# Kernel tuning notes

Hardware: AMD Instinct MI355X
Metric: run time of the kernel (lower is better)

## Reference

```python
import jax, jax.numpy as jnp
import numpy as np

B, L, D, H = 4, 2048, 1024, 16
HD = D // H

def setup_inputs() -> dict:
    key = jax.random.key(0)
    k1, k2, k3, k4 = jax.random.split(key, 4)
    return {
        "Q": jax.random.normal(k1, (B, L, D), dtype=jnp.float32),
        "K": jax.random.normal(k2, (B, L, D), dtype=jnp.float32),
        "V": jax.random.normal(k3, (B, L, D), dtype=jnp.float32),
        "W_out": jax.random.normal(k4, (D, D), dtype=jnp.float32) * (1.0 / np.sqrt(D)),
        "b_out": jnp.zeros((D,), dtype=jnp.float32),
    }

def reference(Q, K, V, W_out, b_out):
    b, l, d = Q.shape
    h, hd = H, d // H
    q = Q.reshape(b, l, h, hd)
    k = K.reshape(b, l, h, hd)
    v = V.reshape(b, l, h, hd)
    # energy: [b, h, q, k]
    energy = jnp.einsum('nqhd,nkhd->nhqk', q, k)
    # NOTE: original scales by sqrt(embed_dim), not sqrt(head_dim)
    attn = jax.nn.softmax(energy / jnp.sqrt(jnp.float32(d)), axis=-1)
    out = jnp.einsum('nhql,nlhd->nqhd', attn, v).reshape(b, l, d)
    # torch nn.Linear: x @ W.T + b
    return out @ W_out.T + b_out
```

## Files before the change

### kernel.cpp

```cpp
#include <hip/hip_runtime.h>
#include <hip/hip_bf16.h>


#define B_  4
#define L_  2048
#define D_  1024
#define H_  16
#define HD_ 64

typedef float  f32x4  __attribute__((ext_vector_type(4)));
typedef short  bf16x8 __attribute__((ext_vector_type(8)));
typedef short  bf16x4 __attribute__((ext_vector_type(4)));

__device__ inline unsigned short f2bf(float x) {
    union { float f; unsigned u; } v; v.f = x;
    unsigned r = v.u + 0x7FFFu + ((v.u >> 16) & 1u);
    return (unsigned short)(r >> 16);
}
__device__ inline unsigned short f2bf_trunc(float x) {
    union { float f; unsigned u; } v; v.f = x;
    return (unsigned short)(v.u >> 16);
}
__device__ inline unsigned pack_trunc2(float lo, float hi) {
    union { float f; unsigned u; } a, b; a.f = lo; b.f = hi;
    return (a.u >> 16) | (b.u & 0xFFFF0000u);
}
__device__ inline float fast_exp2(float x) {
#if __has_builtin(__builtin_amdgcn_exp2f)
    return __builtin_amdgcn_exp2f(x);
#else
    return exp2f(x);
#endif
}
__device__ inline bf16x8 pack8s(float4 a, float4 b, float s) {
    bf16x8 r;
    r[0] = (short)f2bf(a.x * s); r[1] = (short)f2bf(a.y * s);
    r[2] = (short)f2bf(a.z * s); r[3] = (short)f2bf(a.w * s);
    r[4] = (short)f2bf(b.x * s); r[5] = (short)f2bf(b.y * s);
    r[6] = (short)f2bf(b.z * s); r[7] = (short)f2bf(b.w * s);
    return r;
}
__device__ inline void gld16(const void* g, void* l) {
    __builtin_amdgcn_global_load_lds(
        (const __attribute__((address_space(1))) void*)g,
        (__attribute__((address_space(3))) void*)l, 16, 0, 0);
}

__global__ __launch_bounds__(256) void convw_kernel(const float* __restrict__ W,
                                                    unsigned short* __restrict__ Wb) {
    int i = (blockIdx.x * 256 + threadIdx.x) * 4;
    float4 v = *(const float4*)&W[i];
    bf16x4 o;
    o[0] = (short)f2bf(v.x); o[1] = (short)f2bf(v.y);
    o[2] = (short)f2bf(v.z); o[3] = (short)f2bf(v.w);
    *(bf16x4*)&Wb[i] = o;
}

__global__ __launch_bounds__(256, 4) void attn_kernel(const float* __restrict__ Qg,
                                                      const float* __restrict__ Kg,
                                                      const float* __restrict__ Vg,
                                                      unsigned short* __restrict__ Og) {
    __shared__ unsigned short Ks[64 * 72];
    __shared__ unsigned short Vt[64 * 72];
    __shared__ unsigned short Pw[4 * 32 * 72];

    const int tid  = threadIdx.x;
    const int w    = tid >> 6;
    const int lane = tid & 63;
    const int l16  = lane & 15;
    const int quad = lane >> 4;

    const int x   = blockIdx.x;
    const int idx = x >> 3;
    const int bh  = (x & 7) * 8 + (idx & 7);
    const int qb  = idx >> 3;
    const int bz  = bh >> 4;
    const int h   = bh & 15;
    const int q0  = qb * 128;

    const float qscale = 0.04508422f;
    bf16x8 aq[2][2];
    #pragma unroll
    for (int qt = 0; qt < 2; ++qt) {
        const int qrow = q0 + w * 32 + qt * 16 + l16;
        const float* qp = Qg + ((size_t)(bz * L_ + qrow)) * D_ + h * HD_ + quad * 8;
        aq[qt][0] = pack8s(*(const float4*)qp,        *(const float4*)(qp + 4),  qscale);
        aq[qt][1] = pack8s(*(const float4*)(qp + 32), *(const float4*)(qp + 36), qscale);
    }

    f32x4 o[2][4];
    float lsum[2][4];
    #pragma unroll
    for (int qt = 0; qt < 2; ++qt)
        #pragma unroll
        for (int i = 0; i < 4; ++i) {
            o[qt][i] = (f32x4){0.f, 0.f, 0.f, 0.f};
            lsum[qt][i] = 0.f;
        }

    for (int k0 = 0; k0 < L_; k0 += 64) {
        __syncthreads();
        #pragma unroll
        for (int i = 0; i < 4; ++i) {
            int fi  = i * 256 + tid;
            int row = fi >> 4, c4 = fi & 15;
            const float* kp = Kg + ((size_t)(bz * L_ + k0 + row)) * D_ + h * HD_ + c4 * 4;
            float4 kv = *(const float4*)kp;
            bf16x4 kb;
            kb[0] = (short)f2bf(kv.x); kb[1] = (short)f2bf(kv.y);
            kb[2] = (short)f2bf(kv.z); kb[3] = (short)f2bf(kv.w);
            *(bf16x4*)&Ks[row * 72 + c4 * 4] = kb;
        }
        {
            int kp2 = tid & 31, dg = tid >> 5;
            const float* vp = Vg + ((size_t)(bz * L_ + k0 + 2 * kp2)) * D_ + h * HD_ + dg * 8;
            float4 a0 = *(const float4*)vp,        a1 = *(const float4*)(vp + 4);
            float4 b0 = *(const float4*)(vp + D_), b1 = *(const float4*)(vp + D_ + 4);
            const float* aa = (const float*)&a0;
            const float* bb = (const float*)&b0;
            #pragma unroll
            for (int j = 0; j < 4; ++j) {
                *(unsigned*)&Vt[(dg * 8 + j) * 72 + 2 * kp2]       = pack_trunc2(a0[j==0?0:j==1?1:j==2?2:3], b0[j==0?0:j==1?1:j==2?2:3]);
            }
            #pragma unroll
            for (int j = 0; j < 4; ++j) {
                *(unsigned*)&Vt[(dg * 8 + 4 + j) * 72 + 2 * kp2]   = pack_trunc2(((const float*)&a1)[j], ((const float*)&b1)[j]);
            }
            (void)aa; (void)bb;
        }
        __syncthreads();

        #pragma unroll
        for (int qt = 0; qt < 2; ++qt) {
            f32x4 s[4];
            #pragma unroll
            for (int i = 0; i < 4; ++i) s[i] = (f32x4){0.f, 0.f, 0.f, 0.f};
            #pragma unroll
            for (int nt = 0; nt < 4; ++nt)
                #pragma unroll
                for (int ks = 0; ks < 2; ++ks) {
                    bf16x8 kb = *(const bf16x8*)&Ks[(nt * 16 + l16) * 72 + ks * 32 + quad * 8];
                    s[nt] = __builtin_amdgcn_mfma_f32_16x16x32_bf16(aq[qt][ks], kb, s[nt], 0, 0, 0);
                }
            #pragma unroll
            for (int nt = 0; nt < 4; ++nt)
                #pragma unroll
                for (int r = 0; r < 4; ++r) {
                    float p = fast_exp2(s[nt][r]);
                    lsum[qt][r] += p;
                    Pw[(w * 32 + qt * 16 + quad * 4 + r) * 72 + nt * 16 + l16] = f2bf_trunc(p);
                }
        }
        #pragma unroll
        for (int qt = 0; qt < 2; ++qt) {
            bf16x8 pa0 = *(const bf16x8*)&Pw[(w * 32 + qt * 16 + l16) * 72 + quad * 8];
            bf16x8 pa1 = *(const bf16x8*)&Pw[(w * 32 + qt * 16 + l16) * 72 + 32 + quad * 8];
            #pragma unroll
            for (int dt = 0; dt < 4; ++dt) {
                bf16x8 v0 = *(const bf16x8*)&Vt[(dt * 16 + l16) * 72 + quad * 8];
                bf16x8 v1 = *(const bf16x8*)&Vt[(dt * 16 + l16) * 72 + 32 + quad * 8];
                o[qt][dt] = __builtin_amdgcn_mfma_f32_16x16x32_bf16(pa0, v0, o[qt][dt], 0, 0, 0);
                o[qt][dt] = __builtin_amdgcn_mfma_f32_16x16x32_bf16(pa1, v1, o[qt][dt], 0, 0, 0);
            }
        }
    }

    #pragma unroll
    for (int qt = 0; qt < 2; ++qt)
        #pragma unroll
        for (int r = 0; r < 4; ++r) {
            float v = lsum[qt][r];
            #pragma unroll
            for (int m = 1; m < 16; m <<= 1) v += __shfl_xor(v, m);
            lsum[qt][r] = v;
        }

    #pragma unroll
    for (int qt = 0; qt < 2; ++qt)
        #pragma unroll
        for (int r = 0; r < 4; ++r) {
            float inv = 1.0f / lsum[qt][r];
            int q = q0 + w * 32 + qt * 16 + quad * 4 + r;
            #pragma unroll
            for (int dt = 0; dt < 4; ++dt)
                Og[((size_t)(bz * L_ + q)) * D_ + h * HD_ + dt * 16 + l16] =
                    f2bf(o[qt][dt][r] * inv);
        }
}

__global__ __launch_bounds__(256, 2) void proj_kernel(const unsigned short* __restrict__ Og,
                                                      const unsigned short* __restrict__ Wb,
                                                      const float* __restrict__ bias,
                                                      float* __restrict__ Yg) {
    __shared__ unsigned short As[128 * 32];
    __shared__ unsigned short Bs[128 * 32];

    const int tid  = threadIdx.x;
    const int w    = tid >> 6;
    const int lane = tid & 63;
    const int l16  = lane & 15;
    const int quad = lane >> 4;
    const int wm   = w & 1, wn = w >> 1;

    const int m0 = blockIdx.x * 128;
    const int n0 = blockIdx.y * 128;

    f32x4 acc[4][4];
    #pragma unroll
    for (int i = 0; i < 4; ++i)
        #pragma unroll
        for (int j = 0; j < 4; ++j) acc[i][j] = (f32x4){0.f, 0.f, 0.f, 0.f};

    for (int kt = 0; kt < 1024; kt += 32) {
        __syncthreads();
        #pragma unroll
        for (int i = 0; i < 2; ++i) {
            int c   = (i * 4 + w) * 64 + lane;
            int row = c >> 2, q4 = c & 3;
            gld16(&Og[(size_t)(m0 + row) * 1024 + kt + q4 * 8],
                  (char*)As + (size_t)(i * 4 + w) * 1024);
            gld16(&Wb[(size_t)(n0 + row) * 1024 + kt + q4 * 8],
                  (char*)Bs + (size_t)(i * 4 + w) * 1024);
        }
        __syncthreads();

        bf16x8 a[4], b[4];
        #pragma unroll
        for (int mt = 0; mt < 4; ++mt)
            a[mt] = *(const bf16x8*)&As[(wm * 64 + mt * 16 + l16) * 32 + quad * 8];
        #pragma unroll
        for (int nt = 0; nt < 4; ++nt)
            b[nt] = *(const bf16x8*)&Bs[(wn * 64 + nt * 16 + l16) * 32 + quad * 8];
        #pragma unroll
        for (int mt = 0; mt < 4; ++mt)
            #pragma unroll
            for (int nt = 0; nt < 4; ++nt)
                acc[mt][nt] = __builtin_amdgcn_mfma_f32_16x16x32_bf16(a[mt], b[nt], acc[mt][nt], 0, 0, 0);
    }

    #pragma unroll
    for (int mt = 0; mt < 4; ++mt)
        #pragma unroll
        for (int nt = 0; nt < 4; ++nt) {
            int e = n0 + wn * 64 + nt * 16 + l16;
            float bv = bias[e];
            #pragma unroll
            for (int r = 0; r < 4; ++r) {
                int m = m0 + wm * 64 + mt * 16 + quad * 4 + r;
                Yg[(size_t)m * 1024 + e] = acc[mt][nt][r] + bv;
            }
        }
}

extern "C" void kernel_launch(void* const* d_in, const int* in_sizes, int n_in,
                              void* d_out, int out_size, void* d_ws, size_t ws_size,
                              hipStream_t stream) {
    const float* Q    = (const float*)d_in[0];
    const float* K    = (const float*)d_in[1];
    const float* V    = (const float*)d_in[2];
    const float* W    = (const float*)d_in[3];
    const float* bias = (const float*)d_in[4];
    float* Y = (float*)d_out;

    unsigned short* Og = (unsigned short*)d_ws;
    unsigned short* Wb = (unsigned short*)((char*)d_ws + (size_t)16 * 1024 * 1024);

    convw_kernel<<<D_ * D_ / (256 * 4), 256, 0, stream>>>(W, Wb);
    attn_kernel<<<B_ * H_ * (L_ / 128), 256, 0, stream>>>(Q, K, V, Og);
    dim3 pg(B_ * L_ / 128, D_ / 128);
    proj_kernel<<<pg, 256, 0, stream>>>(Og, Wb, bias, Y);
}
```

Baseline: 287.6 us.

## Preconvert K/V to swizzled bf16 and double-buffer async LDS loads in attention and projection

Adds prepass kernels that convert K to bf16 with an XOR-swizzled layout and V to a transposed, swizzled bf16 layout, staged in the output buffer as scratch. The attention kernel then streams these tiles with global_load_lds into double-buffered, unpadded LDS, overlapping the next tile's load with compute and dropping one barrier per iteration. It also computes S transposed so the row sum reduces with fewer shuffles and P is written as packed pairs. The projection GEMM gets the same double buffering. This removes the per-block fp32 to bf16 conversion of K/V, which was repeated for every query block, at the cost of extra prepass launches and extra global traffic.

```diff
diff --git a/kernel.cpp b/kernel.cpp
--- a/kernel.cpp
+++ b/kernel.cpp
@@ -6,7 +6,6 @@
 #define L_  2048
 #define D_  1024
 #define H_  16
-#define HD_ 64
 
 typedef float  f32x4  __attribute__((ext_vector_type(4)));
 typedef short  bf16x8 __attribute__((ext_vector_type(8)));
@@ -17,9 +16,8 @@
     unsigned r = v.u + 0x7FFFu + ((v.u >> 16) & 1u);
     return (unsigned short)(r >> 16);
 }
-__device__ inline unsigned short f2bf_trunc(float x) {
-    union { float f; unsigned u; } v; v.f = x;
-    return (unsigned short)(v.u >> 16);
+__device__ inline unsigned pack_rne2(float lo, float hi) {
+    return (unsigned)f2bf(lo) | ((unsigned)f2bf(hi) << 16);
 }
 __device__ inline unsigned pack_trunc2(float lo, float hi) {
     union { float f; unsigned u; } a, b; a.f = lo; b.f = hi;
@@ -56,13 +54,54 @@
     *(bf16x4*)&Wb[i] = o;
 }
 
-__global__ __launch_bounds__(256, 4) void attn_kernel(const float* __restrict__ Qg,
-                                                      const float* __restrict__ Kg,
-                                                      const float* __restrict__ Vg,
+__global__ __launch_bounds__(256) void convk_kernel(const float* __restrict__ K,
+                                                    unsigned short* __restrict__ Kb) {
+    int o = blockIdx.x * 256 + threadIdx.x;
+    int d8 = o & 7; int h = (o >> 3) & 15; int key = (o >> 7) & 2047; int b = o >> 18;
+    size_t base = ((size_t)(b * L_ + key) * H_ + h) * 64;
+    const float* p = K + base + d8 * 8;
+    float4 a = *(const float4*)p, c = *(const float4*)(p + 4);
+    bf16x8 r;
+    r[0] = (short)f2bf(a.x); r[1] = (short)f2bf(a.y); r[2] = (short)f2bf(a.z); r[3] = (short)f2bf(a.w);
+    r[4] = (short)f2bf(c.x); r[5] = (short)f2bf(c.y); r[6] = (short)f2bf(c.z); r[7] = (short)f2bf(c.w);
+    *(bf16x8*)&Kb[base + ((d8 * 8) ^ ((key & 7) * 8))] = r;
+}
+
+__global__ __launch_bounds__(256) void convv_kernel(const float* __restrict__ V,
+                                                    unsigned short* __restrict__ Vb) {
+    __shared__ unsigned short T[64 * 80];
+    int tid = threadIdx.x;
+    int kb_ = blockIdx.x & 31, bh = blockIdx.x >> 5;
+    int b = bh >> 4, h = bh & 15, k0 = kb_ * 64;
+    int key2 = tid & 31, dg = tid >> 5;
+    const float* pa = V + ((size_t)(b * L_ + k0 + 2 * key2) * H_ + h) * 64 + dg * 8;
+    const float* pb = pa + H_ * 64;
+    float4 a0 = *(const float4*)pa, a1 = *(const float4*)(pa + 4);
+    float4 b0 = *(const float4*)pb, b1 = *(const float4*)(pb + 4);
+    #pragma unroll
+    for (int j = 0; j < 4; ++j)
+        *(unsigned*)&T[(dg * 8 + j) * 80 + 2 * key2] =
+            pack_rne2(((const float*)&a0)[j], ((const float*)&b0)[j]);
+    #pragma unroll
+    for (int j = 0; j < 4; ++j)
+        *(unsigned*)&T[(dg * 8 + 4 + j) * 80 + 2 * key2] =
+            pack_rne2(((const float*)&a1)[j], ((const float*)&b1)[j]);
+    __syncthreads();
+    #pragma unroll
+    for (int i = 0; i < 2; ++i) {
+        int c = i * 256 + tid; int d = c >> 3, ch = c & 7;
+        bf16x8 v = *(const bf16x8*)&T[d * 80 + ch * 8];
+        *(bf16x8*)&Vb[((size_t)(b * H_ + h) * 64 + d) * L_ + k0 + ((ch ^ (d & 7)) * 8)] = v;
+    }
+}
+
+__global__ __launch_bounds__(256, 3) void attn_kernel(const float* __restrict__ Qg,
+                                                      const unsigned short* __restrict__ Kb,
+                                                      const unsigned short* __restrict__ Vb,
                                                       unsigned short* __restrict__ Og) {
-    __shared__ unsigned short Ks[64 * 72];
-    __shared__ unsigned short Vt[64 * 72];
-    __shared__ unsigned short Pw[4 * 32 * 72];
+    __shared__ unsigned short Ks[2][64 * 64];
+    __shared__ unsigned short Vt[2][64 * 64];
+    __shared__ unsigned short Pw[4][32 * 64];
 
     const int tid  = threadIdx.x;
     const int w    = tid >> 6;
@@ -83,108 +122,108 @@
     #pragma unroll
     for (int qt = 0; qt < 2; ++qt) {
         const int qrow = q0 + w * 32 + qt * 16 + l16;
-        const float* qp = Qg + ((size_t)(bz * L_ + qrow)) * D_ + h * HD_ + quad * 8;
+        const float* qp = Qg + ((size_t)(bz * L_ + qrow)) * D_ + h * 64 + quad * 8;
         aq[qt][0] = pack8s(*(const float4*)qp,        *(const float4*)(qp + 4),  qscale);
         aq[qt][1] = pack8s(*(const float4*)(qp + 32), *(const float4*)(qp + 36), qscale);
     }
 
     f32x4 o[2][4];
-    float lsum[2][4];
+    float lsum[2] = {0.f, 0.f};
     #pragma unroll
     for (int qt = 0; qt < 2; ++qt)
         #pragma unroll
-        for (int i = 0; i < 4; ++i) {
-            o[qt][i] = (f32x4){0.f, 0.f, 0.f, 0.f};
-            lsum[qt][i] = 0.f;
-        }
-
-    for (int k0 = 0; k0 < L_; k0 += 64) {
+        for (int i = 0; i < 4; ++i) o[qt][i] = (f32x4){0.f, 0.f, 0.f, 0.f};
+
+    const unsigned short* Kbh = Kb + ((size_t)bz * L_ * H_ + h) * 64;
+    const unsigned short* Vbh = Vb + (size_t)(bz * H_ + h) * 64 * L_;
+    unsigned short* PwF = &Pw[0][0];
+    const int sw = (l16 & 7) * 8;
+
+    #define ISSUE(T, BUF)                                                           \
+        {                                                                           \
+            int k0_ = (T) * 64;                                                     \
+            _Pragma("unroll")                                                       \
+            for (int i = 0; i < 2; ++i) {                                           \
+                int c = i * 256 + tid; int rr = c >> 3, jj = c & 7;                 \
+                gld16(Kbh + (size_t)(k0_ + rr) * (H_ * 64) + jj * 8,                \
+                      (char*)Ks[BUF] + (i * 256 + w * 64) * 16);                    \
+                gld16(Vbh + (size_t)rr * L_ + k0_ + jj * 8,                         \
+                      (char*)Vt[BUF] + (i * 256 + w * 64) * 16);                    \
+            }                                                                       \
+        }
+
+    ISSUE(0, 0)
+
+    for (int t = 0; t < 32; ++t) {
         __syncthreads();
-        #pragma unroll
-        for (int i = 0; i < 4; ++i) {
-            int fi  = i * 256 + tid;
-            int row = fi >> 4, c4 = fi & 15;
-            const float* kp = Kg + ((size_t)(bz * L_ + k0 + row)) * D_ + h * HD_ + c4 * 4;
-            float4 kv = *(const float4*)kp;
-            bf16x4 kb;
-            kb[0] = (short)f2bf(kv.x); kb[1] = (short)f2bf(kv.y);
-            kb[2] = (short)f2bf(kv.z); kb[3] = (short)f2bf(kv.w);
-            *(bf16x4*)&Ks[row * 72 + c4 * 4] = kb;
-        }
-        {
-            int kp2 = tid & 31, dg = tid >> 5;
-            const float* vp = Vg + ((size_t)(bz * L_ + k0 + 2 * kp2)) * D_ + h * HD_ + dg * 8;
-            float4 a0 = *(const float4*)vp,        a1 = *(const float4*)(vp + 4);
-            float4 b0 = *(const float4*)(vp + D_), b1 = *(const float4*)(vp + D_ + 4);
-            const float* aa = (const float*)&a0;
-            const float* bb = (const float*)&b0;
-            #pragma unroll
-            for (int j = 0; j < 4; ++j) {
-                *(unsigned*)&Vt[(dg * 8 + j) * 72 + 2 * kp2]       = pack_trunc2(a0[j==0?0:j==1?1:j==2?2:3], b0[j==0?0:j==1?1:j==2?2:3]);
+        if (t < 31) ISSUE(t + 1, (t + 1) & 1)
+        const unsigned short* ks = Ks[t & 1];
+        const unsigned short* vt = Vt[t & 1];
+
+        f32x4 s[2][4];
+        #pragma unroll
+        for (int nt = 0; nt < 4; ++nt) {
+            bf16x8 k0f = *(const bf16x8*)&ks[(nt * 16 + l16) * 64 + ((quad * 8) ^ sw)];
+            bf16x8 k1f = *(const bf16x8*)&ks[(nt * 16 + l16) * 64 + ((32 + quad * 8) ^ sw)];
+            #pragma unroll
+            for (int qt = 0; qt < 2; ++qt) {
+                f32x4 z = (f32x4){0.f, 0.f, 0.f, 0.f};
+                z = __builtin_amdgcn_mfma_f32_16x16x32_bf16(k0f, aq[qt][0], z, 0, 0, 0);
+                s[qt][nt] = __builtin_amdgcn_mfma_f32_16x16x32_bf16(k1f, aq[qt][1], z, 0, 0, 0);
             }
-            #pragma unroll
-            for (int j = 0; j < 4; ++j) {
-                *(unsigned*)&Vt[(dg * 8 + 4 + j) * 72 + 2 * kp2]   = pack_trunc2(((const float*)&a1)[j], ((const float*)&b1)[j]);
+        }
+
+        #pragma unroll
+        for (int qt = 0; qt < 2; ++qt) {
+            int prow = (w * 32 + qt * 16 + l16) * 64;
+            #pragma unroll
+            for (int nt = 0; nt < 4; ++nt) {
+                float p0 = fast_exp2(s[qt][nt][0]), p1 = fast_exp2(s[qt][nt][1]);
+                float p2 = fast_exp2(s[qt][nt][2]), p3 = fast_exp2(s[qt][nt][3]);
+                lsum[qt] += (p0 + p1) + (p2 + p3);
+                int cb = nt * 16 + quad * 4;
+                *(unsigned*)&PwF[prow + ((cb)     ^ sw)] = pack_trunc2(p0, p1);
+                *(unsigned*)&PwF[prow + ((cb + 2) ^ sw)] = pack_trunc2(p2, p3);
             }
-            (void)aa; (void)bb;
-        }
-        __syncthreads();
-
+        }
+
+        bf16x8 pav[2][2];
         #pragma unroll
         for (int qt = 0; qt < 2; ++qt) {
-            f32x4 s[4];
-            #pragma unroll
-            for (int i = 0; i < 4; ++i) s[i] = (f32x4){0.f, 0.f, 0.f, 0.f};
-            #pragma unroll
-            for (int nt = 0; nt < 4; ++nt)
-                #pragma unroll
-                for (int ks = 0; ks < 2; ++ks) {
-                    bf16x8 kb = *(const bf16x8*)&Ks[(nt * 16 + l16) * 72 + ks * 32 + quad * 8];
-                    s[nt] = __builtin_amdgcn_mfma_f32_16x16x32_bf16(aq[qt][ks], kb, s[nt], 0, 0, 0);
-                }
-            #pragma unroll
-            for (int nt = 0; nt < 4; ++nt)
-                #pragma unroll
-                for (int r = 0; r < 4; ++r) {
-                    float p = fast_exp2(s[nt][r]);
-                    lsum[qt][r] += p;
-                    Pw[(w * 32 + qt * 16 + quad * 4 + r) * 72 + nt * 16 + l16] = f2bf_trunc(p);
-                }
-        }
-        #pragma unroll
-        for (int qt = 0; qt < 2; ++qt) {
-            bf16x8 pa0 = *(const bf16x8*)&Pw[(w * 32 + qt * 16 + l16) * 72 + quad * 8];
-            bf16x8 pa1 = *(const bf16x8*)&Pw[(w * 32 + qt * 16 + l16) * 72 + 32 + quad * 8];
-            #pragma unroll
-            for (int dt = 0; dt < 4; ++dt) {
-                bf16x8 v0 = *(const bf16x8*)&Vt[(dt * 16 + l16) * 72 + quad * 8];
-                bf16x8 v1 = *(const bf16x8*)&Vt[(dt * 16 + l16) * 72 + 32 + quad * 8];
-                o[qt][dt] = __builtin_amdgcn_mfma_f32_16x16x32_bf16(pa0, v0, o[qt][dt], 0, 0, 0);
-                o[qt][dt] = __builtin_amdgcn_mfma_f32_16x16x32_bf16(pa1, v1, o[qt][dt], 0, 0, 0);
+            int prow = (w * 32 + qt * 16 + l16) * 64;
+            pav[qt][0] = *(const bf16x8*)&PwF[prow + ((quad * 8)      ^ sw)];
+            pav[qt][1] = *(const bf16x8*)&PwF[prow + ((32 + quad * 8) ^ sw)];
+        }
+        #pragma unroll
+        for (int dt = 0; dt < 4; ++dt) {
+            bf16x8 v0 = *(const bf16x8*)&vt[(dt * 16 + l16) * 64 + ((quad * 8)      ^ sw)];
+            bf16x8 v1 = *(const bf16x8*)&vt[(dt * 16 + l16) * 64 + ((32 + quad * 8) ^ sw)];
+            #pragma unroll
+            for (int qt = 0; qt < 2; ++qt) {
+                o[qt][dt] = __builtin_amdgcn_mfma_f32_16x16x32_bf16(pav[qt][0], v0, o[qt][dt], 0, 0, 0);
+                o[qt][dt] = __builtin_amdgcn_mfma_f32_16x16x32_bf16(pav[qt][1], v1, o[qt][dt], 0, 0, 0);
             }
         }
     }
 
+    float tot[2];
+    #pragma unroll
+    for (int qt = 0; qt < 2; ++qt) {
+        float v = lsum[qt];
+        v += __shfl_xor(v, 16); v += __shfl_xor(v, 32);
+        tot[qt] = v;
+    }
     #pragma unroll
     for (int qt = 0; qt < 2; ++qt)
         #pragma unroll
         for (int r = 0; r < 4; ++r) {
-            float v = lsum[qt][r];
-            #pragma unroll
-            for (int m = 1; m < 16; m <<= 1) v += __shfl_xor(v, m);
-            lsum[qt][r] = v;
-        }
-
-    #pragma unroll
-    for (int qt = 0; qt < 2; ++qt)
-        #pragma unroll
-        for (int r = 0; r < 4; ++r) {
-            float inv = 1.0f / lsum[qt][r];
+            float tv  = __shfl(tot[qt], quad * 4 + r);
+            float inv = 1.0f / tv;
             int q = q0 + w * 32 + qt * 16 + quad * 4 + r;
+            size_t rowb = ((size_t)(bz * L_ + q)) * D_ + h * 64;
             #pragma unroll
             for (int dt = 0; dt < 4; ++dt)
-                Og[((size_t)(bz * L_ + q)) * D_ + h * HD_ + dt * 16 + l16] =
-                    f2bf(o[qt][dt][r] * inv);
+                Og[rowb + dt * 16 + l16] = f2bf(o[qt][dt][r] * inv);
         }
 }
 
@@ -192,8 +231,8 @@
                                                       const unsigned short* __restrict__ Wb,
                                                       const float* __restrict__ bias,
                                                       float* __restrict__ Yg) {
-    __shared__ unsigned short As[128 * 32];
-    __shared__ unsigned short Bs[128 * 32];
+    __shared__ unsigned short As[2][128 * 32];
+    __shared__ unsigned short Bs[2][128 * 32];
 
     const int tid  = threadIdx.x;
     const int w    = tid >> 6;
@@ -211,26 +250,34 @@
         #pragma unroll
         for (int j = 0; j < 4; ++j) acc[i][j] = (f32x4){0.f, 0.f, 0.f, 0.f};
 
-    for (int kt = 0; kt < 1024; kt += 32) {
+    #define PISSUE(T, BUF)                                                          \
+        {                                                                           \
+            int kt_ = (T) * 32;                                                     \
+            _Pragma("unroll")                                                       \
+            for (int i = 0; i < 2; ++i) {                                           \
+                int c = i * 256 + tid; int row = c >> 2, q4 = c & 3;                \
+                gld16(&Og[(size_t)(m0 + row) * 1024 + kt_ + q4 * 8],                \
+                      (char*)As[BUF] + (i * 256 + w * 64) * 16);                    \
+                gld16(&Wb[(size_t)(n0 + row) * 1024 + kt_ + q4 * 8],                \
+                      (char*)Bs[BUF] + (i * 256 + w * 64) * 16);                    \
+            }                                                                       \
+        }
+
+    PISSUE(0, 0)
+
+    for (int t = 0; t < 32; ++t) {
         __syncthreads();
-        #pragma unroll
-        for (int i = 0; i < 2; ++i) {
-            int c   = (i * 4 + w) * 64 + lane;
-            int row = c >> 2, q4 = c & 3;
-            gld16(&Og[(size_t)(m0 + row) * 1024 + kt + q4 * 8],
-                  (char*)As + (size_t)(i * 4 + w) * 1024);
-            gld16(&Wb[(size_t)(n0 + row) * 1024 + kt + q4 * 8],
-                  (char*)Bs + (size_t)(i * 4 + w) * 1024);
-        }
-        __syncthreads();
+        if (t < 31) PISSUE(t + 1, (t + 1) & 1)
+        const unsigned short* as = As[t & 1];
+        const unsigned short* bs = Bs[t & 1];
 
         bf16x8 a[4], b[4];
         #pragma unroll
         for (int mt = 0; mt < 4; ++mt)
-            a[mt] = *(const bf16x8*)&As[(wm * 64 + mt * 16 + l16) * 32 + quad * 8];
+            a[mt] = *(const bf16x8*)&as[(wm * 64 + mt * 16 + l16) * 32 + quad * 8];
         #pragma unroll
         for (int nt = 0; nt < 4; ++nt)
-            b[nt] = *(const bf16x8*)&Bs[(wn * 64 + nt * 16 + l16) * 32 + quad * 8];
+            b[nt] = *(const bf16x8*)&bs[(wn * 64 + nt * 16 + l16) * 32 + quad * 8];
         #pragma unroll
         for (int mt = 0; mt < 4; ++mt)
             #pragma unroll
@@ -264,9 +311,13 @@
 
     unsigned short* Og = (unsigned short*)d_ws;
     unsigned short* Wb = (unsigned short*)((char*)d_ws + (size_t)16 * 1024 * 1024);
+    unsigned short* Kb = (unsigned short*)d_out;
+    unsigned short* Vb = Kb + (size_t)B_ * H_ * L_ * 64;
 
     convw_kernel<<<D_ * D_ / (256 * 4), 256, 0, stream>>>(W, Wb);
-    attn_kernel<<<B_ * H_ * (L_ / 128), 256, 0, stream>>>(Q, K, V, Og);
+    convk_kernel<<<B_ * L_ * H_ * 8 / 256, 256, 0, stream>>>(K, Kb);
+    convv_kernel<<<B_ * H_ * (L_ / 64), 256, 0, stream>>>(V, Vb);
+    attn_kernel<<<B_ * H_ * (L_ / 128), 256, 0, stream>>>(Q, Kb, Vb, Og);
     dim3 pg(B_ * L_ / 128, D_ / 128);
     proj_kernel<<<pg, 256, 0, stream>>>(Og, Wb, bias, Y);
 }
```

Result: faster. 265.9 us (-7.5%).
